# Optimization experiments

Hardware: AMD Instinct MI355X
Metric: run time of the kernel (lower is better)

The kernel has to match this reference:

```python
import jax, jax.numpy as jnp
import numpy as np

N_NODES = 100000
N_EDGES = 200000
B_GRAPHS = 128
H = 8
DC = 256
DE = 124           # dim_embedding; node features are DE + 4 = 128
DV = 64


def setup_inputs() -> dict:
    key = jax.random.key(0)
    ks = jax.random.split(key, 10)

    def unif(k, shape):
        stdv = 1.0 / np.sqrt(shape[-1])
        return jax.random.uniform(k, shape, jnp.float32, -stdv, stdv)

    x = jax.random.normal(ks[0], (N_NODES, DE + 4), jnp.float32)
    edge_index = jax.random.randint(ks[1], (2, N_EDGES), 0, N_NODES)
    batch = jnp.sort(jax.random.randint(ks[2], (N_NODES,), 0, B_GRAPHS))
    context = jax.random.normal(ks[3], (B_GRAPHS, DC), jnp.float32)
    Wq = unif(ks[4], (H, DC, DV))
    Wk = unif(ks[5], (H, DE + 4, DV))
    Wv = unif(ks[6], (H, DE + 4, DV))
    query_coef = unif(ks[7], (1,))
    Wf = unif(ks[8], (DV, DE))
    return {"x": x, "edge_index": edge_index, "batch": batch, "context": context,
            "Wq": Wq, "Wk": Wk, "Wv": Wv, "query_coef": query_coef, "Wf": Wf}


def reference(x, edge_index, batch, context, Wq, Wk, Wv, query_coef, Wf):
    # edge_index is unused by the original forward.
    n_heads, _, dv = Wq.shape
    n_graphs = context.shape[0]

    query = jnp.einsum('bc,hcv->hbv', context, Wq)       # [H, B, Dv]
    keys = jnp.einsum('ne,hev->hnv', x, Wk)              # [H, N, Dv]
    values = jnp.einsum('ne,hev->hnv', x, Wv)            # [H, N, Dv]

    # original builds u = keys @ query^T [H,N,B] then gathers u[h,n,batch[n]];
    # compute only the gathered per-node score directly (same math).
    q_node = query[:, batch, :]                          # [H, N, Dv]
    u = jnp.sum(keys * q_node, axis=-1) / jnp.sqrt(jnp.asarray(dv, x.dtype))  # [H, N]

    # segment softmax per head over nodes of each graph
    seg_max = jax.vmap(lambda s: jax.ops.segment_max(s, batch, num_segments=n_graphs))(u)
    e = jnp.exp(u - seg_max[:, batch])                   # [H, N]
    seg_sum = jax.vmap(lambda s: jax.ops.segment_sum(s, batch, num_segments=n_graphs))(e)
    a = e / (seg_sum[:, batch] + 1e-16)                  # [H, N]

    v = a[..., None] * values                            # [H, N, Dv]
    agg = jax.vmap(lambda s: jax.ops.segment_sum(s, batch, num_segments=n_graphs))(v)  # [H, B, Dv]

    h = query_coef * query + agg                         # [H, B, Dv]
    h = jnp.einsum('hbv,ve->hbe', h, Wf)                 # [H, B, De]
    return jnp.sum(h, axis=0)                            # [B, De]
```

## Files before the change

### kernel.cpp

```cpp
#include <hip/hip_runtime.h>

#define N_NODES 100000
#define B_GRAPHS 128
#define H_HEADS 8
#define DC 256
#define DF 128
#define DV 64
#define DE 124
#define SPLITS 16
#define GROUPS 8
#define PART_STRIDE (H_HEADS * DF + H_HEADS)


__device__ __forceinline__ float red32(float v) {
  v += __int_as_float(__builtin_amdgcn_update_dpp(0, __float_as_int(v), 0xB1,  0xF, 0xF, true));
  v += __int_as_float(__builtin_amdgcn_update_dpp(0, __float_as_int(v), 0x4E,  0xF, 0xF, true));
  v += __int_as_float(__builtin_amdgcn_update_dpp(0, __float_as_int(v), 0x141, 0xF, 0xF, true));
  v += __int_as_float(__builtin_amdgcn_update_dpp(0, __float_as_int(v), 0x140, 0xF, 0xF, true));
  v += __int_as_float(__builtin_amdgcn_ds_swizzle(__float_as_int(v), 0x401f));
  return v;
}

__global__ __launch_bounds__(256) void k_prep(
    const float* __restrict__ context, const float* __restrict__ Wq,
    const float* __restrict__ Wk, const int* __restrict__ batch,
    float* __restrict__ query_ws, float* __restrict__ kq_ws, int* __restrict__ starts)
{
  const int b = blockIdx.x;
  const int t = threadIdx.x;
  __shared__ float ctxs[DC];
  __shared__ float qs[H_HEADS * DV];
  ctxs[t] = context[b * DC + t];
  if (t < 32) {
    const int l = t;
    int lo = 0, len = N_NODES;
    while (len > 1) {
      const int chunk = (len + 31) >> 5;
      const int idx = lo + l * chunk;
      const bool lt = (idx < lo + len) && (idx < N_NODES) && (batch[idx] < b);
      const unsigned mh = (unsigned)(__ballot(lt) & 0xffffffffu);
      const int k = __popc(mh);
      if (k == 0) break;
      lo += (k - 1) * chunk + 1;
      len = chunk;
    }
    if (l == 0) {
      starts[b] = lo;
      if (b == 0) starts[B_GRAPHS] = N_NODES;
    }
  }
  __syncthreads();
  if (t < H_HEADS * DV / 4) {
    const int h = t >> 4, v4 = (t & 15) * 4;
    const float4* wq = reinterpret_cast<const float4*>(Wq + (size_t)h * DC * DV + v4);
    float4 acc = make_float4(0.f, 0.f, 0.f, 0.f);
    for (int c = 0; c < DC; ++c) {
      const float4 w = wq[c * (DV / 4)];
      const float cc = ctxs[c];
      acc.x += cc * w.x; acc.y += cc * w.y; acc.z += cc * w.z; acc.w += cc * w.w;
    }
    *reinterpret_cast<float4*>(qs + h * DV + v4) = acc;
    *reinterpret_cast<float4*>(query_ws + (h * B_GRAPHS + b) * DV + v4) = acc;
  }
  __syncthreads();
  for (int i = t; i < H_HEADS * DF; i += 256) {
    const int h = i >> 7;
    const float4* wk = reinterpret_cast<const float4*>(Wk + (size_t)i * DV);
    const float4* q4 = reinterpret_cast<const float4*>(qs + h * DV);
    float acc = 0.f;
    #pragma unroll
    for (int v4 = 0; v4 < DV / 4; ++v4) {
      const float4 a = wk[v4], q = q4[v4];
      acc += a.x * q.x + a.y * q.y + a.z * q.z + a.w * q.w;
    }
    kq_ws[(h * B_GRAPHS + b) * DF + (i & 127)] = acc * 0.125f;
  }
}

__global__ __launch_bounds__(256) void k_main(
    const float* __restrict__ x, const float* __restrict__ kq_ws,
    const int* __restrict__ starts, float* __restrict__ partials)
{
  const int bid = blockIdx.x;
  const int g = bid >> 4, sp = bid & 15;
  const int t = threadIdx.x;
  const int grp = t >> 5, l32 = t & 31;
  const int s0 = starts[g], s1 = starts[g + 1];
  const int len = s1 - s0;
  const int i0 = s0 + (len * sp) / SPLITS;
  const int i1 = s0 + (len * (sp + 1)) / SPLITS;

  float4 kqr[H_HEADS];
  #pragma unroll
  for (int h = 0; h < H_HEADS; ++h)
    kqr[h] = *reinterpret_cast<const float4*>(kq_ws + (h * B_GRAPHS + g) * DF + 4 * l32);

  float4 s[H_HEADS];
  float l[H_HEADS];
  #pragma unroll
  for (int h = 0; h < H_HEADS; ++h) { s[h] = make_float4(0.f, 0.f, 0.f, 0.f); l[h] = 0.f; }

  int n = i0 + grp;
  float4 a0 = make_float4(0.f, 0.f, 0.f, 0.f);
  float4 a1 = make_float4(0.f, 0.f, 0.f, 0.f);
  if (n < i1)          a0 = *reinterpret_cast<const float4*>(x + (size_t)n * DF + 4 * l32);
  if (n + GROUPS < i1) a1 = *reinterpret_cast<const float4*>(x + (size_t)(n + GROUPS) * DF + 4 * l32);
  while (n < i1) {
    float4 a2 = make_float4(0.f, 0.f, 0.f, 0.f);
    if (n + 2 * GROUPS < i1)
      a2 = *reinterpret_cast<const float4*>(x + (size_t)(n + 2 * GROUPS) * DF + 4 * l32);
    float u[H_HEADS];
    #pragma unroll
    for (int h = 0; h < H_HEADS; ++h)
      u[h] = a0.x * kqr[h].x + a0.y * kqr[h].y + a0.z * kqr[h].z + a0.w * kqr[h].w;
    #pragma unroll
    for (int h = 0; h < H_HEADS; ++h) u[h] = red32(u[h]);
    #pragma unroll
    for (int h = 0; h < H_HEADS; ++h) {
      const float e = __expf(u[h]);
      l[h] += e;
      s[h].x += e * a0.x; s[h].y += e * a0.y; s[h].z += e * a0.z; s[h].w += e * a0.w;
    }
    a0 = a1; a1 = a2; n += GROUPS;
  }

  __shared__ float sbuf[4][H_HEADS * DF];
  __shared__ float lbuf[GROUPS][H_HEADS];
  if (l32 == 0) {
    #pragma unroll
    for (int h = 0; h < H_HEADS; ++h) lbuf[grp][h] = l[h];
  }
  if (grp >= 4) {
    #pragma unroll
    for (int h = 0; h < H_HEADS; ++h)
      *reinterpret_cast<float4*>(&sbuf[grp - 4][h * DF + 4 * l32]) = s[h];
  }
  __syncthreads();
  if (grp < 4) {
    #pragma unroll
    for (int h = 0; h < H_HEADS; ++h) {
      const float4 o = *reinterpret_cast<const float4*>(&sbuf[grp][h * DF + 4 * l32]);
      s[h].x += o.x; s[h].y += o.y; s[h].z += o.z; s[h].w += o.w;
    }
  }
  __syncthreads();
  if (grp < 4) {
    #pragma unroll
    for (int h = 0; h < H_HEADS; ++h)
      *reinterpret_cast<float4*>(&sbuf[grp][h * DF + 4 * l32]) = s[h];
  }
  __syncthreads();
  float* part = partials + (size_t)bid * PART_STRIDE;
  for (int i = t; i < H_HEADS * DF; i += 256) {
    float acc = 0.f;
    #pragma unroll
    for (int gq = 0; gq < 4; ++gq) acc += sbuf[gq][i];
    part[i] = acc;
  }
  if (t < H_HEADS) {
    float acc = 0.f;
    #pragma unroll
    for (int gq = 0; gq < GROUPS; ++gq) acc += lbuf[gq][t];
    part[H_HEADS * DF + t] = acc;
  }
}

__global__ __launch_bounds__(256) void k_final(
    const float* __restrict__ partials, const float* __restrict__ query_ws,
    const float* __restrict__ Wv, const float* __restrict__ Wf,
    const float* __restrict__ qcoef, float* __restrict__ out)
{
  const int g = blockIdx.x;
  const int t = threadIdx.x;
  __shared__ float w[H_HEADS * DF];
  __shared__ float lg[H_HEADS];
  __shared__ float Gp[4][DV];
  const float* part = partials + (size_t)g * SPLITS * PART_STRIDE;
  if (t < H_HEADS) {
    float acc = 0.f;
    #pragma unroll
    for (int sp = 0; sp < SPLITS; ++sp) acc += part[sp * PART_STRIDE + H_HEADS * DF + t];
    lg[t] = acc;
  }
  __syncthreads();
  for (int i = t; i < H_HEADS * DF; i += 256) {
    float acc = 0.f;
    #pragma unroll
    for (int sp = 0; sp < SPLITS; ++sp) acc += part[sp * PART_STRIDE + i];
    w[i] = acc / (lg[i >> 7] + 1e-16f);
  }
  __syncthreads();
  const float qc = qcoef[0];
  const int v = t & 63, p = t >> 6;
  float acc = qc * (query_ws[((2 * p) * B_GRAPHS + g) * DV + v] +
                    query_ws[((2 * p + 1) * B_GRAPHS + g) * DV + v]);
  #pragma unroll
  for (int hh = 2 * p; hh <= 2 * p + 1; ++hh) {
    const float* wv = Wv + ((size_t)hh * DF) * DV + v;
    const float* wh = w + hh * DF;
    for (int e = 0; e < DF; ++e) acc += wh[e] * wv[(size_t)e * DV];
  }
  Gp[p][v] = acc;
  __syncthreads();
  if (t < DE) {
    float o = 0.f;
    for (int v2 = 0; v2 < DV; ++v2) {
      const float Gv = Gp[0][v2] + Gp[1][v2] + Gp[2][v2] + Gp[3][v2];
      o += Gv * Wf[v2 * DE + t];
    }
    out[g * DE + t] = o;
  }
}

extern "C" void kernel_launch(void* const* d_in, const int* in_sizes, int n_in,
                              void* d_out, int out_size, void* d_ws, size_t ws_size,
                              hipStream_t stream) {
  const float* x       = (const float*)d_in[0];
  const int*   batch   = (const int*)d_in[2];
  const float* context = (const float*)d_in[3];
  const float* Wq      = (const float*)d_in[4];
  const float* Wk      = (const float*)d_in[5];
  const float* Wv      = (const float*)d_in[6];
  const float* qc      = (const float*)d_in[7];
  const float* Wf      = (const float*)d_in[8];
  float* out = (float*)d_out;

  float* ws       = (float*)d_ws;
  float* query_ws = ws;
  float* kq_ws    = ws + 65536;
  float* partials = ws + 196608;
  int*   starts   = (int*)(ws + 196608 + B_GRAPHS * SPLITS * PART_STRIDE);

  hipLaunchKernelGGL(k_prep, dim3(B_GRAPHS), dim3(256), 0, stream,
                     context, Wq, Wk, batch, query_ws, kq_ws, starts);
  hipLaunchKernelGGL(k_main, dim3(B_GRAPHS * SPLITS), dim3(256), 0, stream,
                     x, kq_ws, starts, partials);
  hipLaunchKernelGGL(k_final, dim3(B_GRAPHS), dim3(256), 0, stream,
                     partials, query_ws, Wv, Wf, qc, out);
}
```

Measured before the change: 144.2 us.

## Split prep kernel across head pairs, stage kq in LDS, fold log2e into scale

The prep kernel now launches four blocks per graph, each computing two heads, with the context-by-Wq reduction split across two thread halves. This spreads the small query and key-query projections over more blocks to cut prep latency. The main kernel stages the key-query vectors in shared memory instead of holding eight float4 in registers, which lowers register pressure at the cost of LDS reads inside the loop. The score scale now includes log2(e), so the loop can use exp2f in place of __expf.

Measured after the change: 141.4 us. Within noise of the previous version (-1.9%).

```diff
diff --git a/kernel.cpp b/kernel.cpp
--- a/kernel.cpp
+++ b/kernel.cpp
@@ -1,4 +1,5 @@
 #include <hip/hip_runtime.h>
+#include <math.h>
 
 #define N_NODES 100000
 #define B_GRAPHS 128
@@ -10,6 +11,7 @@
 #define SPLITS 16
 #define GROUPS 8
 #define PART_STRIDE (H_HEADS * DF + H_HEADS)
+#define KQ_SCALE 0.18033688011112042f
 
 
 __device__ __forceinline__ float red32(float v) {
@@ -26,17 +28,17 @@
     const float* __restrict__ Wk, const int* __restrict__ batch,
     float* __restrict__ query_ws, float* __restrict__ kq_ws, int* __restrict__ starts)
 {
-  const int b = blockIdx.x;
+  const int b = blockIdx.x >> 2, hp = blockIdx.x & 3;
   const int t = threadIdx.x;
   __shared__ float ctxs[DC];
-  __shared__ float qs[H_HEADS * DV];
+  __shared__ float qpart[256];
+  __shared__ float qs[2 * DV];
   ctxs[t] = context[b * DC + t];
-  if (t < 32) {
-    const int l = t;
+  if (hp == 0 && t < 32) {
     int lo = 0, len = N_NODES;
     while (len > 1) {
       const int chunk = (len + 31) >> 5;
-      const int idx = lo + l * chunk;
+      const int idx = lo + t * chunk;
       const bool lt = (idx < lo + len) && (idx < N_NODES) && (batch[idx] < b);
       const unsigned mh = (unsigned)(__ballot(lt) & 0xffffffffu);
       const int k = __popc(mh);
@@ -44,36 +46,43 @@
       lo += (k - 1) * chunk + 1;
       len = chunk;
     }
-    if (l == 0) {
+    if (t == 0) {
       starts[b] = lo;
       if (b == 0) starts[B_GRAPHS] = N_NODES;
     }
   }
   __syncthreads();
-  if (t < H_HEADS * DV / 4) {
-    const int h = t >> 4, v4 = (t & 15) * 4;
-    const float4* wq = reinterpret_cast<const float4*>(Wq + (size_t)h * DC * DV + v4);
-    float4 acc = make_float4(0.f, 0.f, 0.f, 0.f);
-    for (int c = 0; c < DC; ++c) {
-      const float4 w = wq[c * (DV / 4)];
-      const float cc = ctxs[c];
-      acc.x += cc * w.x; acc.y += cc * w.y; acc.z += cc * w.z; acc.w += cc * w.w;
-    }
-    *reinterpret_cast<float4*>(qs + h * DV + v4) = acc;
-    *reinterpret_cast<float4*>(query_ws + (h * B_GRAPHS + b) * DV + v4) = acc;
-  }
-  __syncthreads();
-  for (int i = t; i < H_HEADS * DF; i += 256) {
-    const int h = i >> 7;
-    const float4* wk = reinterpret_cast<const float4*>(Wk + (size_t)i * DV);
-    const float4* q4 = reinterpret_cast<const float4*>(qs + h * DV);
+  {
+    const int o = t & 127, half = t >> 7;
+    const int hl = o >> 6, v = o & 63;
+    const int h = 2 * hp + hl;
+    const float* wq = Wq + (size_t)h * DC * DV + v;
+    float acc = 0.f;
+    #pragma unroll 4
+    for (int c = half * 128; c < half * 128 + 128; ++c) acc += ctxs[c] * wq[(size_t)c * DV];
+    qpart[t] = acc;
+  }
+  __syncthreads();
+  if (t < 128) {
+    const int hl = t >> 6, v = t & 63;
+    const int h = 2 * hp + hl;
+    const float q = qpart[t] + qpart[t + 128];
+    qs[t] = q;
+    query_ws[(h * B_GRAPHS + b) * DV + v] = q;
+  }
+  __syncthreads();
+  {
+    const int hl = t >> 7, e = t & 127;
+    const int h = 2 * hp + hl;
+    const float4* wk = reinterpret_cast<const float4*>(Wk + ((size_t)h * DF + e) * DV);
+    const float4* q4 = reinterpret_cast<const float4*>(qs + hl * DV);
     float acc = 0.f;
     #pragma unroll
     for (int v4 = 0; v4 < DV / 4; ++v4) {
       const float4 a = wk[v4], q = q4[v4];
       acc += a.x * q.x + a.y * q.y + a.z * q.z + a.w * q.w;
     }
-    kq_ws[(h * B_GRAPHS + b) * DF + (i & 127)] = acc * 0.125f;
+    kq_ws[(h * B_GRAPHS + b) * DF + e] = acc * KQ_SCALE;
   }
 }
 
@@ -85,15 +94,22 @@
   const int g = bid >> 4, sp = bid & 15;
   const int t = threadIdx.x;
   const int grp = t >> 5, l32 = t & 31;
+
+  __shared__ float kqs[H_HEADS * DF];
+  __shared__ float sbuf[4][H_HEADS * DF];
+  __shared__ float lbuf[GROUPS][H_HEADS];
+
+  {
+    const float4* src = reinterpret_cast<const float4*>(kq_ws);
+    const int h = t >> 5, q4 = t & 31;
+    reinterpret_cast<float4*>(kqs)[h * 32 + q4] = src[((h * B_GRAPHS + g) * DF >> 2) + q4];
+  }
   const int s0 = starts[g], s1 = starts[g + 1];
+  __syncthreads();
+
   const int len = s1 - s0;
   const int i0 = s0 + (len * sp) / SPLITS;
   const int i1 = s0 + (len * (sp + 1)) / SPLITS;
-
-  float4 kqr[H_HEADS];
-  #pragma unroll
-  for (int h = 0; h < H_HEADS; ++h)
-    kqr[h] = *reinterpret_cast<const float4*>(kq_ws + (h * B_GRAPHS + g) * DF + 4 * l32);
 
   float4 s[H_HEADS];
   float l[H_HEADS];
@@ -111,21 +127,21 @@
       a2 = *reinterpret_cast<const float4*>(x + (size_t)(n + 2 * GROUPS) * DF + 4 * l32);
     float u[H_HEADS];
     #pragma unroll
-    for (int h = 0; h < H_HEADS; ++h)
-      u[h] = a0.x * kqr[h].x + a0.y * kqr[h].y + a0.z * kqr[h].z + a0.w * kqr[h].w;
+    for (int h = 0; h < H_HEADS; ++h) {
+      const float4 k4 = *reinterpret_cast<const float4*>(&kqs[h * DF + 4 * l32]);
+      u[h] = a0.x * k4.x + a0.y * k4.y + a0.z * k4.z + a0.w * k4.w;
+    }
     #pragma unroll
     for (int h = 0; h < H_HEADS; ++h) u[h] = red32(u[h]);
     #pragma unroll
     for (int h = 0; h < H_HEADS; ++h) {
-      const float e = __expf(u[h]);
+      const float e = exp2f(u[h]);
       l[h] += e;
       s[h].x += e * a0.x; s[h].y += e * a0.y; s[h].z += e * a0.z; s[h].w += e * a0.w;
     }
     a0 = a1; a1 = a2; n += GROUPS;
   }
 
-  __shared__ float sbuf[4][H_HEADS * DF];
-  __shared__ float lbuf[GROUPS][H_HEADS];
   if (l32 == 0) {
     #pragma unroll
     for (int h = 0; h < H_HEADS; ++h) lbuf[grp][h] = l[h];
@@ -231,7 +247,7 @@
   float* partials = ws + 196608;
   int*   starts   = (int*)(ws + 196608 + B_GRAPHS * SPLITS * PART_STRIDE);
 
-  hipLaunchKernelGGL(k_prep, dim3(B_GRAPHS), dim3(256), 0, stream,
+  hipLaunchKernelGGL(k_prep, dim3(B_GRAPHS * 4), dim3(256), 0, stream,
                      context, Wq, Wk, batch, query_ws, kq_ws, starts);
   hipLaunchKernelGGL(k_main, dim3(B_GRAPHS * SPLITS), dim3(256), 0, stream,
                      x, kq_ws, starts, partials);
```
